# Kernel tuning notes

Hardware: AMD Instinct MI355X
Metric: run time of the kernel (lower is better)

## Reference

```python
import jax, jax.numpy as jnp
import numpy as np

# Pangu-Weather EarthAttention3D, dim=192 branch
H = 6                 # heads
D = 192               # dim
DH = D // H           # head dim = 32
N = 2 * 6 * 12        # window tokens = 144
TW = (8 // 2) * (186 // 6)  # type_of_windows = 124
NW = 8                # number of windows (leading batch axis)
SCALE = DH ** -0.5


def setup_inputs() -> dict:
    key = jax.random.key(0)
    ks = jax.random.split(key, 7)
    return {
        "x": jax.random.normal(ks[0], (NW, TW, N, D), jnp.float32),
        "mask": jax.random.normal(ks[1], (NW, TW, N, N), jnp.float32),
        "w_qkv": jax.random.normal(ks[2], (D, 3 * D), jnp.float32) * 0.02,
        "b_qkv": jnp.zeros((3 * D,), jnp.float32),
        "bias": jax.random.normal(ks[3], (1, TW, H, N, N), jnp.float32) * 0.02,
        "w_out": jax.random.normal(ks[4], (D, D), jnp.float32) * 0.02,
        "b_out": jnp.zeros((D,), jnp.float32),
    }


def reference(x, mask, w_qkv, b_qkv, bias, w_out, b_out):
    B, W, Ntok, Dm = x.shape  # (nW, type_of_windows, win_tokens, dim)
    # fused QKV projection
    qkv = (x @ w_qkv + b_qkv).reshape(B, W, Ntok, 3, H, DH)
    qkv = jnp.transpose(qkv, (3, 0, 1, 4, 2, 5))  # (3, B, W, H, N, dh)
    q, k, v = qkv[0] * SCALE, qkv[1], qkv[2]
    # scores + earth-specific bias + window mask (broadcast over heads)
    attn = jnp.einsum('bwhnd,bwhmd->bwhnm', q, k)
    attn = attn + bias + mask[:, :, None, :, :]
    attn = jax.nn.softmax(attn, axis=-1)  # dropout_rate=0 -> identity
    out = jnp.einsum('bwhnm,bwhmd->bwhnd', attn, v)
    out = jnp.transpose(out, (0, 1, 3, 2, 4)).reshape(B, W, Ntok, Dm)
    return out @ w_out + b_out
```

## Files before the change

kernel.cpp:

```cpp
#include <hip/hip_runtime.h>
#include <hip/hip_bf16.h>

typedef __bf16 bf16_t;
typedef bf16_t bf16x8 __attribute__((ext_vector_type(8)));
typedef bf16_t bf16x4 __attribute__((ext_vector_type(4)));
typedef float f32x4 __attribute__((ext_vector_type(4)));

#define SCALE 0.17677669529663687f

#define PIN(x) asm volatile("" : "+v"(x))

__device__ __forceinline__ int swz_elem(int r, int c) {
    int g = c >> 3;
    return r * 192 + ((g >> 3) << 6) + (((g & 7) ^ (r & 7)) << 3) + (c & 7);
}

__device__ __forceinline__ void stage_chunk(bf16_t* dst, const bf16_t* src, int tid) {
#pragma unroll
    for (int it = 0; it < 3; ++it) {
        int off = (it * 256 + tid) * 8;
        __builtin_amdgcn_global_load_lds(
            (const __attribute__((address_space(1))) unsigned int*)(src + off),
            (__attribute__((address_space(3))) unsigned int*)(dst + off),
            16, 0, 0);
    }
}

__device__ __forceinline__ void stage_1k(bf16_t* dst, const bf16_t* src, int lane) {
    __builtin_amdgcn_global_load_lds(
        (const __attribute__((address_space(1))) unsigned int*)(src + lane * 8),
        (__attribute__((address_space(3))) unsigned int*)(dst + lane * 8),
        16, 0, 0);
}

__global__ void prep_weights(const float* __restrict__ w_qkv, const float* __restrict__ w_out,
                             bf16_t* __restrict__ wqkvS, bf16_t* __restrict__ woutS) {
    int i = blockIdx.x * 256 + threadIdx.x;
    if (i < 576 * 192) {
        int o = i / 192, k = i % 192;
        float v = w_qkv[k * 576 + o];
        if (o < 192) v *= SCALE;
        wqkvS[(o >> 5) * 6144 + swz_elem(o & 31, k)] = (bf16_t)v;
    }
    if (i < 192 * 192) {
        int o = i / 192, k = i % 192;
        woutS[(o >> 5) * 6144 + swz_elem(o & 31, k)] = (bf16_t)w_out[k * 192 + o];
    }
}

__global__ __launch_bounds__(256, 8)
void prep_bm2(const float* __restrict__ bias, const float* __restrict__ mask,
              bf16_t* __restrict__ biasP, bf16_t* __restrict__ maskP)
{
    __shared__ bf16_t L[16 * 148];
    int blk = blockIdx.x;
    bool isMask = blk >= 6696;
    int region = isMask ? blk - 6696 : blk;
    int rg = region / 9, t = region % 9;
    const float* src = (isMask ? mask : bias) + ((size_t)rg * 144 + t * 16) * 144;
    bf16_t* dst = (isMask ? maskP : biasP) + (size_t)region * 2560;
    const int tid = threadIdx.x;

    for (int i = tid; i < 576; i += 256) {
        int row = i / 36, seg = i % 36;
        f32x4 v = *(const f32x4*)(src + row * 144 + seg * 4);
        bf16x4 o;
        o[0] = (bf16_t)v[0]; o[1] = (bf16_t)v[1]; o[2] = (bf16_t)v[2]; o[3] = (bf16_t)v[3];
        *(bf16x4*)&L[row * 148 + seg * 4] = o;
    }
    __syncthreads();

    for (int u = tid; u < 320; u += 256) {
        int it = u >> 6, lane = u & 63;
        int lrow = lane & 15, lgrp = lane >> 4;
        bf16x8 o;
#pragma unroll
        for (int e = 0; e < 8; ++e) {
            int us = it * 8 + e;
            int nt = us >> 2, j = us & 3;
            int m = (us < 36) ? (nt * 16 + lgrp * 4 + j) : 0;
            bf16_t v = L[lrow * 148 + m];
            o[e] = (us < 36) ? v : (bf16_t)0.f;
        }
        *(bf16x8*)(dst + it * 512 + lane * 8) = o;
    }
}

__global__ __launch_bounds__(256, 4)
void qkv_gemm(const float* __restrict__ x, const float* __restrict__ b_qkv,
              const bf16_t* __restrict__ wqkvS,
              bf16_t* __restrict__ Qg, bf16_t* __restrict__ Kg, bf16_t* __restrict__ Vt)
{
    __shared__ __align__(16) bf16_t Wb[2][6144];
    __shared__ __align__(16) bf16_t T[4][1280];
    const int tid  = threadIdx.x;
    const int lane = tid & 63;
    const int wave = tid >> 6;
    const int lrow = lane & 15;
    const int lgrp = lane >> 4;
    const int r0   = blockIdx.x * 128 + wave * 32;

    stage_chunk(&Wb[0][0], wqkvS, tid);

    bf16x8 af[2][6];
#pragma unroll
    for (int tt = 0; tt < 2; ++tt)
#pragma unroll
        for (int ks = 0; ks < 6; ++ks) {
            const float* px = x + (size_t)(r0 + tt * 16 + lrow) * 192 + ks * 32 + lgrp * 8;
            f32x4 lo = *(const f32x4*)px;
            f32x4 hi = *(const f32x4*)(px + 4);
            bf16x8 v;
            v[0] = (bf16_t)lo[0]; v[1] = (bf16_t)lo[1]; v[2] = (bf16_t)lo[2]; v[3] = (bf16_t)lo[3];
            v[4] = (bf16_t)hi[0]; v[5] = (bf16_t)hi[1]; v[6] = (bf16_t)hi[2]; v[7] = (bf16_t)hi[3];
            af[tt][ks] = v;
        }
    __syncthreads();

    bf16_t* tl = &T[wave][0];

    for (int hc = 0; hc < 18; ++hc) {
        if (hc < 17) stage_chunk(&Wb[(hc + 1) & 1][0], wqkvS + (hc + 1) * 6144, tid);
        const bf16_t* wb = &Wb[hc & 1][0];

        f32x4 a[2][2];
        a[0][0] = f32x4{0.f,0.f,0.f,0.f}; a[0][1] = f32x4{0.f,0.f,0.f,0.f};
        a[1][0] = f32x4{0.f,0.f,0.f,0.f}; a[1][1] = f32x4{0.f,0.f,0.f,0.f};
#pragma unroll
        for (int ks = 0; ks < 6; ++ks) {
            bf16x8 wf0 = *(const bf16x8*)&wb[swz_elem(lrow,      ks * 32 + lgrp * 8)];
            bf16x8 wf1 = *(const bf16x8*)&wb[swz_elem(16 + lrow, ks * 32 + lgrp * 8)];
#pragma unroll
            for (int tt = 0; tt < 2; ++tt) {
                a[tt][0] = __builtin_amdgcn_mfma_f32_16x16x32_bf16(af[tt][ks], wf0, a[tt][0], 0, 0, 0);
                a[tt][1] = __builtin_amdgcn_mfma_f32_16x16x32_bf16(af[tt][ks], wf1, a[tt][1], 0, 0, 0);
            }
        }
        __syncthreads();

        float b0 = b_qkv[hc * 32 + lrow], b1 = b_qkv[hc * 32 + 16 + lrow];
        if (hc < 6) { b0 *= SCALE; b1 *= SCALE; }

        if (hc < 12) {
            const int h = (hc < 6) ? hc : hc - 6;
            bf16_t* dst = (hc < 6) ? Qg : Kg;
#pragma unroll
            for (int tt = 0; tt < 2; ++tt) {
#pragma unroll
                for (int j = 0; j < 4; ++j) {
                    tl[tt * 640 + (lgrp * 4 + j) * 40 + lrow]      = (bf16_t)(a[tt][0][j] + b0);
                    tl[tt * 640 + (lgrp * 4 + j) * 40 + 16 + lrow] = (bf16_t)(a[tt][1][j] + b1);
                }
                bf16x8 val = *(const bf16x8*)&tl[tt * 640 + lrow * 40 + lgrp * 8];
                int tk = r0 + tt * 16 + lrow, bw = tk / 144, n = tk % 144;
                *(bf16x8*)&dst[((size_t)(bw * 6 + h) * 144 + n) * 32 + lgrp * 8] = val;
            }
        } else {
            const int hv = hc - 12;
#pragma unroll
            for (int tt = 0; tt < 2; ++tt)
#pragma unroll
                for (int j = 0; j < 4; ++j) {
                    tl[(lrow) * 40      + tt * 16 + lgrp * 4 + j] = (bf16_t)(a[tt][0][j] + b0);
                    tl[(16 + lrow) * 40 + tt * 16 + lgrp * 4 + j] = (bf16_t)(a[tt][1][j] + b1);
                }
#pragma unroll
            for (int it = 0; it < 2; ++it) {
                int slot = it * 64 + lane;
                int d = slot >> 2, c = slot & 3;
                int tk = r0 + c * 8, bw = tk / 144, n = tk % 144;
                bf16x8 val = *(const bf16x8*)&tl[d * 40 + c * 8];
                *(bf16x8*)&Vt[((size_t)(bw * 6 + hv) * 32 + d) * 160 + n] = val;
            }
        }
    }
}

__global__ __launch_bounds__(192, 3)
void earth_attn_v10(const bf16_t* __restrict__ Qg, const bf16_t* __restrict__ Kg,
                    const bf16_t* __restrict__ Vt,
                    const bf16_t* __restrict__ maskP, const bf16_t* __restrict__ biasP,
                    bf16_t* __restrict__ Og)
{
    __shared__ __align__(16) bf16_t Kl[4608];
    __shared__ __align__(16) bf16_t Vl[5120];
    __shared__ __align__(16) bf16_t P[3][16 * 168];
    const int tid  = threadIdx.x;
    const int lane = tid & 63;
    const int wave = tid >> 6;
    const int lrow = lane & 15;
    const int lgrp = lane >> 4;

    const int orig = blockIdx.x;
    const int blk  = (orig & 7) * 744 + (orig >> 3);

    const int ww = blk / 48;
    const int r1 = blk % 48;
    const int b  = r1 / 6;
    const int h  = r1 % 6;
    const int bw = b * 124 + ww;

    const size_t kbase = ((size_t)(bw * 6 + h) * 144) * 32;
    const size_t vbase = ((size_t)(bw * 6 + h) * 32) * 160;

    for (int c = wave; c < 9; c += 3)  stage_1k(Kl + c * 512, Kg + kbase + c * 512, lane);
    for (int c = wave; c < 10; c += 3) stage_1k(Vl + c * 512, Vt + vbase + c * 512, lane);

    bf16_t* pb = &P[wave][0];
    {
        uint2 z2 = make_uint2(0u, 0u);
        *(uint2*)&pb[lrow * 168 + 144 + lgrp * 4] = z2;
    }
    __syncthreads();

    const bf16_t* bpB = biasP + (size_t)(ww * 6 + h) * 9 * 2560 + lane * 8;
    const bf16_t* mpB = maskP + (size_t)bw * 9 * 2560 + lane * 8;
    bf16_t* ogp = Og + ((size_t)bw * 144) * 192 + h * 32 + lgrp * 8;

#pragma unroll 1
    for (int i = 0; i < 3; ++i) {
        const int t = wave + i * 3;

        bf16x8 bvv[5], mvv[5];
#pragma unroll
        for (int it = 0; it < 5; ++it) {
            bvv[it] = *(const bf16x8*)(bpB + (size_t)t * 2560 + it * 512);
            mvv[it] = *(const bf16x8*)(mpB + (size_t)t * 2560 + it * 512);
        }
        bf16x8 qa = *(const bf16x8*)&Qg[kbase + (size_t)(t * 16 + lrow) * 32 + lgrp * 8];

        f32x4 s[9];
#pragma unroll
        for (int nt = 0; nt < 9; ++nt)
#pragma unroll
            for (int j = 0; j < 4; ++j) {
                const int u = nt * 4 + j;
                s[nt][j] = (float)bvv[u >> 3][u & 7] + (float)mvv[u >> 3][u & 7];
            }

#pragma unroll
        for (int nt = 0; nt < 9; ++nt) {
            bf16x8 ka = *(const bf16x8*)&Kl[(nt * 16 + lrow) * 32 + lgrp * 8];
            s[nt] = __builtin_amdgcn_mfma_f32_16x16x32_bf16(ka, qa, s[nt], 0, 0, 0);
        }

        float mx = -1e30f;
#pragma unroll
        for (int nt = 0; nt < 9; ++nt)
#pragma unroll
            for (int j = 0; j < 4; ++j) mx = fmaxf(mx, s[nt][j]);
        mx = fmaxf(mx, __shfl_xor(mx, 16, 64));
        mx = fmaxf(mx, __shfl_xor(mx, 32, 64));
        float sum = 0.f;
#pragma unroll
        for (int nt = 0; nt < 9; ++nt)
#pragma unroll
            for (int j = 0; j < 4; ++j) { float e = __expf(s[nt][j] - mx); s[nt][j] = e; sum += e; }
        sum += __shfl_xor(sum, 16, 64);
        sum += __shfl_xor(sum, 32, 64);
        const float rinv = 1.0f / sum;

#pragma unroll
        for (int nt = 0; nt < 9; ++nt) {
            bf16x4 pw;
#pragma unroll
            for (int j = 0; j < 4; ++j) pw[j] = (bf16_t)(s[nt][j] * rinv);
            *(bf16x4*)&pb[lrow * 168 + nt * 16 + lgrp * 4] = pw;
        }

        f32x4 o0{0.f, 0.f, 0.f, 0.f}, o1{0.f, 0.f, 0.f, 0.f};
#pragma unroll
        for (int ks = 0; ks < 5; ++ks) {
            bf16x8 pa = *(const bf16x8*)&pb[lrow * 168 + ks * 32 + lgrp * 8];
            bf16x8 v0 = *(const bf16x8*)&Vl[lrow * 160 + ks * 32 + lgrp * 8];
            bf16x8 v1 = *(const bf16x8*)&Vl[(16 + lrow) * 160 + ks * 32 + lgrp * 8];
            o0 = __builtin_amdgcn_mfma_f32_16x16x32_bf16(pa, v0, o0, 0, 0, 0);
            o1 = __builtin_amdgcn_mfma_f32_16x16x32_bf16(pa, v1, o1, 0, 0, 0);
        }

#pragma unroll
        for (int j = 0; j < 4; ++j) {
            pb[(lgrp * 4 + j) * 168 + lrow]      = (bf16_t)o0[j];
            pb[(lgrp * 4 + j) * 168 + 16 + lrow] = (bf16_t)o1[j];
        }
        bf16x8 ov = *(const bf16x8*)&pb[lrow * 168 + lgrp * 8];
        *(bf16x8*)(ogp + (size_t)(t * 16 + lrow) * 192) = ov;
    }
}

__global__ __launch_bounds__(256, 2)
void earth_attn_v7(const bf16_t* __restrict__ Qg, const bf16_t* __restrict__ Kg,
                   const bf16_t* __restrict__ Vt,
                   const float* __restrict__ mask, const float* __restrict__ bias,
                   bf16_t* __restrict__ Og)
{
    __shared__ bf16_t P[4][16 * 168];
    const int tid  = threadIdx.x;
    const int lane = tid & 63;
    const int wave = tid >> 6;
    const int lrow = lane & 15;
    const int lgrp = lane >> 4;
    const int orig = blockIdx.x;
    const int blk  = (orig & 7) * 186 + (orig >> 3);
    const int wid = blk * 4 + wave;
    const int ww  = wid / 48;
    const int r1  = wid % 48;
    const int b   = r1 / 6;
    const int h   = r1 % 6;
    const int bw  = b * 124 + ww;
    const size_t kbase = ((size_t)(bw * 6 + h) * 144) * 32;
    const size_t vbase = ((size_t)(bw * 6 + h) * 32) * 160;

    bf16x8 ka[9];
#pragma unroll
    for (int nt = 0; nt < 9; ++nt)
        ka[nt] = *(const bf16x8*)&Kg[kbase + (size_t)(nt * 16 + lrow) * 32 + lgrp * 8];
    bf16x8 va0[5], va1[5];
#pragma unroll
    for (int ks = 0; ks < 5; ++ks) {
        va0[ks] = *(const bf16x8*)&Vt[vbase + (size_t)lrow * 160 + ks * 32 + lgrp * 8];
        va1[ks] = *(const bf16x8*)&Vt[vbase + (size_t)(16 + lrow) * 160 + ks * 32 + lgrp * 8];
    }
    const float* bp_base = bias + (size_t)(ww * 6 + h) * 144 * 144;
    const float* mp_base = mask + (size_t)bw * 144 * 144;
    bf16_t* pb = &P[wave][0];
    bf16_t* ogp = Og + ((size_t)bw * 144) * 192 + h * 32 + lgrp * 8;
    bf16x8 qa = *(const bf16x8*)&Qg[kbase + (size_t)lrow * 32 + lgrp * 8];
    f32x4 bv[9], mv[9];
    {
        const float* bp = bp_base + (size_t)lrow * 144;
        const float* mp = mp_base + (size_t)lrow * 144;
#pragma unroll
        for (int nt = 0; nt < 9; ++nt) {
            bv[nt] = *(const f32x4*)(bp + nt * 16 + lgrp * 4);
            mv[nt] = *(const f32x4*)(mp + nt * 16 + lgrp * 4);
        }
    }
#pragma unroll 1
    for (int t = 0; t < 9; ++t) {
        f32x4 s[9];
#pragma unroll
        for (int nt = 0; nt < 9; ++nt) s[nt] = bv[nt] + mv[nt];
        const int tn = (t < 8) ? t + 1 : 8;
        bf16x8 qa_n = *(const bf16x8*)&Qg[kbase + (size_t)(tn * 16 + lrow) * 32 + lgrp * 8];
        {
            const float* bp = bp_base + (size_t)(tn * 16 + lrow) * 144;
            const float* mp = mp_base + (size_t)(tn * 16 + lrow) * 144;
#pragma unroll
            for (int nt = 0; nt < 9; ++nt) {
                bv[nt] = *(const f32x4*)(bp + nt * 16 + lgrp * 4);
                mv[nt] = *(const f32x4*)(mp + nt * 16 + lgrp * 4);
            }
        }
#pragma unroll
        for (int nt = 0; nt < 9; ++nt)
            s[nt] = __builtin_amdgcn_mfma_f32_16x16x32_bf16(ka[nt], qa, s[nt], 0, 0, 0);
        float mx = -1e30f;
#pragma unroll
        for (int nt = 0; nt < 9; ++nt)
#pragma unroll
            for (int j = 0; j < 4; ++j) mx = fmaxf(mx, s[nt][j]);
        mx = fmaxf(mx, __shfl_xor(mx, 16, 64));
        mx = fmaxf(mx, __shfl_xor(mx, 32, 64));
        float sum = 0.f;
#pragma unroll
        for (int nt = 0; nt < 9; ++nt)
#pragma unroll
            for (int j = 0; j < 4; ++j) { float e = __expf(s[nt][j] - mx); s[nt][j] = e; sum += e; }
        sum += __shfl_xor(sum, 16, 64);
        sum += __shfl_xor(sum, 32, 64);
        const float rinv = 1.0f / sum;
#pragma unroll
        for (int nt = 0; nt < 9; ++nt) {
            bf16x4 pw;
#pragma unroll
            for (int j = 0; j < 4; ++j) pw[j] = (bf16_t)(s[nt][j] * rinv);
            *(bf16x4*)&pb[lrow * 168 + nt * 16 + lgrp * 4] = pw;
        }
        {
            uint2 z2 = make_uint2(0u, 0u);
            *(uint2*)&pb[lrow * 168 + 144 + lgrp * 4] = z2;
        }
        bf16x8 pa[5];
#pragma unroll
        for (int ks = 0; ks < 5; ++ks)
            pa[ks] = *(const bf16x8*)&pb[lrow * 168 + ks * 32 + lgrp * 8];
#pragma unroll
        for (int ks = 0; ks < 5; ++ks) PIN(pa[ks]);
        f32x4 o0{0.f, 0.f, 0.f, 0.f}, o1{0.f, 0.f, 0.f, 0.f};
#pragma unroll
        for (int ks = 0; ks < 5; ++ks) {
            o0 = __builtin_amdgcn_mfma_f32_16x16x32_bf16(pa[ks], va0[ks], o0, 0, 0, 0);
            o1 = __builtin_amdgcn_mfma_f32_16x16x32_bf16(pa[ks], va1[ks], o1, 0, 0, 0);
        }
#pragma unroll
        for (int j = 0; j < 4; ++j) {
            pb[(lgrp * 4 + j) * 168 + lrow]      = (bf16_t)o0[j];
            pb[(lgrp * 4 + j) * 168 + 16 + lrow] = (bf16_t)o1[j];
        }
        bf16x8 ov = *(const bf16x8*)&pb[lrow * 168 + lgrp * 8];
        *(bf16x8*)(ogp + (size_t)(t * 16 + lrow) * 192) = ov;
        qa = qa_n;
    }
}

__global__ __launch_bounds__(256, 4)
void out_proj(const bf16_t* __restrict__ Og, const bf16_t* __restrict__ woutS,
              const float* __restrict__ b_out, float* __restrict__ out)
{
    __shared__ __align__(16) bf16_t Wb[2][6144];
    const int tid  = threadIdx.x;
    const int lane = tid & 63;
    const int wave = tid >> 6;
    const int lrow = lane & 15;
    const int lgrp = lane >> 4;
    const size_t row0 = (size_t)blockIdx.x * 64 + wave * 16;

    stage_chunk(&Wb[0][0], woutS, tid);

    bf16x8 af[6];
#pragma unroll
    for (int ks = 0; ks < 6; ++ks)
        af[ks] = *(const bf16x8*)(Og + (row0 + lrow) * 192 + ks * 32 + lgrp * 8);
    __syncthreads();

#pragma unroll
    for (int c = 0; c < 6; ++c) {
        if (c < 5) stage_chunk(&Wb[(c + 1) & 1][0], woutS + (c + 1) * 6144, tid);
        const bf16_t* wb = &Wb[c & 1][0];
        float b0 = b_out[c * 32 + lrow], b1 = b_out[c * 32 + 16 + lrow];
        f32x4 a0{b0, b0, b0, b0}, a1{b1, b1, b1, b1};
#pragma unroll
        for (int ks = 0; ks < 6; ++ks) {
            bf16x8 wf0 = *(const bf16x8*)&wb[swz_elem(lrow,      ks * 32 + lgrp * 8)];
            bf16x8 wf1 = *(const bf16x8*)&wb[swz_elem(16 + lrow, ks * 32 + lgrp * 8)];
            a0 = __builtin_amdgcn_mfma_f32_16x16x32_bf16(af[ks], wf0, a0, 0, 0, 0);
            a1 = __builtin_amdgcn_mfma_f32_16x16x32_bf16(af[ks], wf1, a1, 0, 0, 0);
        }
        __syncthreads();
#pragma unroll
        for (int j = 0; j < 4; ++j) {
            out[(row0 + lgrp * 4 + j) * 192 + c * 32 + lrow]      = a0[j];
            out[(row0 + lgrp * 4 + j) * 192 + c * 32 + 16 + lrow] = a1[j];
        }
    }
}

extern "C" void kernel_launch(void* const* d_in, const int* in_sizes, int n_in,
                              void* d_out, int out_size, void* d_ws, size_t ws_size,
                              hipStream_t stream) {
    const float* x     = (const float*)d_in[0];
    const float* mask  = (const float*)d_in[1];
    const float* w_qkv = (const float*)d_in[2];
    const float* b_qkv = (const float*)d_in[3];
    const float* bias  = (const float*)d_in[4];
    const float* w_out = (const float*)d_in[5];
    const float* b_out = (const float*)d_in[6];

    bf16_t* wqkvS = (bf16_t*)d_ws;
    bf16_t* woutS = wqkvS + 576 * 192;
    bf16_t* Qg    = woutS + 192 * 192;
    bf16_t* Kg    = Qg + (size_t)992 * 6 * 144 * 32;
    bf16_t* Vt    = Kg + (size_t)992 * 6 * 144 * 32;
    bf16_t* Og    = Vt + (size_t)992 * 6 * 32 * 160;
    bf16_t* biasP = Og + (size_t)992 * 144 * 192;
    bf16_t* maskP = biasP + (size_t)6696 * 2560;

    const size_t need_v10 = ((size_t)112902144 + 17141760 + 22855680) * 2;

    prep_weights<<<dim3(432), dim3(256), 0, stream>>>(w_qkv, w_out, wqkvS, woutS);
    qkv_gemm<<<dim3(1116), dim3(256), 0, stream>>>(x, b_qkv, wqkvS, Qg, Kg, Vt);

    if (ws_size >= need_v10) {
        prep_bm2<<<dim3(15624), dim3(256), 0, stream>>>(bias, mask, biasP, maskP);
        earth_attn_v10<<<dim3(5952), dim3(192), 0, stream>>>(Qg, Kg, Vt, maskP, biasP, Og);
    } else {
        earth_attn_v7<<<dim3(1488), dim3(256), 0, stream>>>(Qg, Kg, Vt, mask, bias, Og);
    }
    out_proj<<<dim3(2232), dim3(256), 0, stream>>>(Og, woutS, b_out, (float*)d_out);
}
```

Measured before the change: 266.1 us.

## Triple-buffer QKV weight staging with per-block chunk rotation and explicit vmcnt waits

The QKV GEMM moves from double to triple buffering of weight chunks in LDS. It waits on partial vmcnt counts and raw s_barrier instead of __syncthreads, so loads stay in flight across iterations. Each block starts at a different weight chunk (blockIdx % 18, and % 6 in out_proj) to spread L2 reads, and the QKV bias is cached in LDS. The hand-counted vmcnt values depend on the exact number of outstanding loads per iteration, including the global stores, so a miscount would race. LDS use rises, which may lower occupancy.

```diff
diff --git a/kernel.cpp b/kernel.cpp
--- a/kernel.cpp
+++ b/kernel.cpp
@@ -91,16 +91,18 @@
               const bf16_t* __restrict__ wqkvS,
               bf16_t* __restrict__ Qg, bf16_t* __restrict__ Kg, bf16_t* __restrict__ Vt)
 {
-    __shared__ __align__(16) bf16_t Wb[2][6144];
+    __shared__ __align__(16) bf16_t Wb[3][6144];
     __shared__ __align__(16) bf16_t T[4][1280];
+    __shared__ float bl[576];
     const int tid  = threadIdx.x;
     const int lane = tid & 63;
     const int wave = tid >> 6;
     const int lrow = lane & 15;
     const int lgrp = lane >> 4;
     const int r0   = blockIdx.x * 128 + wave * 32;
-
-    stage_chunk(&Wb[0][0], wqkvS, tid);
+    const int c0   = blockIdx.x % 18;
+
+    for (int i = tid; i < 576; i += 256) bl[i] = b_qkv[i];
 
     bf16x8 af[2][6];
 #pragma unroll
@@ -115,13 +117,28 @@
             v[4] = (bf16_t)hi[0]; v[5] = (bf16_t)hi[1]; v[6] = (bf16_t)hi[2]; v[7] = (bf16_t)hi[3];
             af[tt][ks] = v;
         }
-    __syncthreads();
+
+    stage_chunk(&Wb[0][0], wqkvS + c0 * 6144, tid);
+    {
+        int nc = c0 + 1; if (nc >= 18) nc -= 18;
+        stage_chunk(&Wb[1][0], wqkvS + nc * 6144, tid);
+    }
+    asm volatile("s_waitcnt vmcnt(3) lgkmcnt(0)" ::: "memory");
+    __builtin_amdgcn_sched_barrier(0);
+    __builtin_amdgcn_s_barrier();
+    __builtin_amdgcn_sched_barrier(0);
 
     bf16_t* tl = &T[wave][0];
 
-    for (int hc = 0; hc < 18; ++hc) {
-        if (hc < 17) stage_chunk(&Wb[(hc + 1) & 1][0], wqkvS + (hc + 1) * 6144, tid);
-        const bf16_t* wb = &Wb[hc & 1][0];
+#pragma unroll 1
+    for (int i = 0; i < 18; ++i) {
+        int hc = c0 + i; if (hc >= 18) hc -= 18;
+
+        if (i <= 15) {
+            int nc = c0 + i + 2; if (nc >= 18) nc -= 18;
+            stage_chunk(&Wb[(i + 2) % 3][0], wqkvS + nc * 6144, tid);
+        }
+        const bf16_t* wb = &Wb[i % 3][0];
 
         f32x4 a[2][2];
         a[0][0] = f32x4{0.f,0.f,0.f,0.f}; a[0][1] = f32x4{0.f,0.f,0.f,0.f};
@@ -136,9 +153,8 @@
                 a[tt][1] = __builtin_amdgcn_mfma_f32_16x16x32_bf16(af[tt][ks], wf1, a[tt][1], 0, 0, 0);
             }
         }
-        __syncthreads();
-
-        float b0 = b_qkv[hc * 32 + lrow], b1 = b_qkv[hc * 32 + 16 + lrow];
+
+        float b0 = bl[hc * 32 + lrow], b1 = bl[hc * 32 + 16 + lrow];
         if (hc < 6) { b0 *= SCALE; b1 *= SCALE; }
 
         if (hc < 12) {
@@ -172,6 +188,15 @@
                 bf16x8 val = *(const bf16x8*)&tl[d * 40 + c * 8];
                 *(bf16x8*)&Vt[((size_t)(bw * 6 + hv) * 32 + d) * 160 + n] = val;
             }
+        }
+
+        if (i < 17) {
+            if (i == 0)       { asm volatile("s_waitcnt vmcnt(5)" ::: "memory"); }
+            else if (i <= 15) { asm volatile("s_waitcnt vmcnt(7)" ::: "memory"); }
+            else              { asm volatile("s_waitcnt vmcnt(4)" ::: "memory"); }
+            __builtin_amdgcn_sched_barrier(0);
+            __builtin_amdgcn_s_barrier();
+            __builtin_amdgcn_sched_barrier(0);
         }
     }
 }
@@ -415,8 +440,9 @@
     const int lrow = lane & 15;
     const int lgrp = lane >> 4;
     const size_t row0 = (size_t)blockIdx.x * 64 + wave * 16;
-
-    stage_chunk(&Wb[0][0], woutS, tid);
+    const int c0   = blockIdx.x % 6;
+
+    stage_chunk(&Wb[0][0], woutS + c0 * 6144, tid);
 
     bf16x8 af[6];
 #pragma unroll
@@ -424,10 +450,14 @@
         af[ks] = *(const bf16x8*)(Og + (row0 + lrow) * 192 + ks * 32 + lgrp * 8);
     __syncthreads();
 
-#pragma unroll
-    for (int c = 0; c < 6; ++c) {
-        if (c < 5) stage_chunk(&Wb[(c + 1) & 1][0], woutS + (c + 1) * 6144, tid);
-        const bf16_t* wb = &Wb[c & 1][0];
+#pragma unroll 1
+    for (int i = 0; i < 6; ++i) {
+        int c = c0 + i; if (c >= 6) c -= 6;
+        if (i < 5) {
+            int nc = c + 1; if (nc >= 6) nc -= 6;
+            stage_chunk(&Wb[(i + 1) & 1][0], woutS + nc * 6144, tid);
+        }
+        const bf16_t* wb = &Wb[i & 1][0];
         float b0 = b_out[c * 32 + lrow], b1 = b_out[c * 32 + 16 + lrow];
         f32x4 a0{b0, b0, b0, b0}, a1{b1, b1, b1, b1};
 #pragma unroll
```

Measured after the change: 259.7 us (median of 2 runs). -2.4%, faster.
